# Optimization experiments

Measured on AMD Instinct MI355X. Metric: run time of the kernel, lower is better.

Reference implementation:

```python
import jax, jax.numpy as jnp
import numpy as np

B = 8192        # batch
OBS = 256       # obs_dim
ACT = 32        # action_dim -> output is 2*ACT (mu, log_std)
HID = 512       # hidden_dim
P = 8           # number of base policies (experts)
LOG_STD_MIN, LOG_STD_MAX = -5.0, 2.0


def setup_inputs() -> dict:
    key = jax.random.key(0)
    ks = jax.random.split(key, 14)
    s = 0.05
    return {
        "obs": jax.random.normal(ks[0], (B, OBS), dtype=jnp.float32),
        # gate network: obs -> HID -> HID -> P (softmax)
        "gw0": jax.random.normal(ks[1], (HID, OBS), dtype=jnp.float32) * s,
        "gb0": jnp.zeros((HID,), dtype=jnp.float32),
        "gw1": jax.random.normal(ks[2], (HID, HID), dtype=jnp.float32) * s,
        "gb1": jnp.zeros((HID,), dtype=jnp.float32),
        "gw2": jax.random.normal(ks[3], (P, HID), dtype=jnp.float32) * s,
        "gb2": jnp.zeros((P,), dtype=jnp.float32),
        # stacked expert (base-policy) trunk params, hidden_depth=2
        "ew0": jax.random.normal(ks[4], (P, HID, OBS), dtype=jnp.float32) * s,
        "eb0": jax.random.normal(ks[5], (P, HID), dtype=jnp.float32) * s,
        "ew1": jax.random.normal(ks[6], (P, HID, HID), dtype=jnp.float32) * s,
        "eb1": jax.random.normal(ks[7], (P, HID), dtype=jnp.float32) * s,
        "ew2": jax.random.normal(ks[8], (P, 2 * ACT, HID), dtype=jnp.float32) * s,
        "eb2": jax.random.normal(ks[9], (P, 2 * ACT), dtype=jnp.float32) * s,
    }


def _blend_linear(blend, W, b, x):
    # Math identical to: W_new = reshape(blend @ flatten(W,1)); bmm(W_new, x) + blend @ b
    # Contracted in the efficient order (per-expert GEMM then blend): [B,P,out] intermediate.
    y = jnp.einsum('bp,poi,bi->bo', blend, W, x, optimize=True)
    return y + blend @ b


def reference(obs, gw0, gb0, gw1, gb1, gw2, gb2, ew0, eb0, ew1, eb1, ew2, eb2):
    # gate network with softmax output
    h = jax.nn.relu(obs @ gw0.T + gb0)
    h = jax.nn.relu(h @ gw1.T + gb1)
    blend = jax.nn.softmax(h @ gw2.T + gb2, axis=-1)  # [B, P]

    # blended per-sample MLP (hidden_depth = 2)
    x = jax.nn.relu(_blend_linear(blend, ew0, eb0, obs))
    x = jax.nn.relu(_blend_linear(blend, ew1, eb1, x))
    x = _blend_linear(blend, ew2, eb2, x)  # [B, 2*ACT]

    mu, log_std = jnp.split(x, 2, axis=-1)
    log_std = jnp.tanh(log_std)
    log_std = LOG_STD_MIN + 0.5 * (LOG_STD_MAX - LOG_STD_MIN) * (log_std + 1.0)
    std = jnp.exp(log_std)
    # dist = SquashedNormal(mu, std); return its defining tensors
    return jnp.concatenate([mu, std], axis=-1)
```

## Files before the change

kernel.cpp:

```cpp
#include <hip/hip_runtime.h>
#include <hip/hip_bf16.h>
#include <cstdint>
#include <cstddef>

#define B_DIM   8192
#define OBS_DIM 256
#define ACT_DIM 32
#define HID_DIM 512
#define NEXPERT 8

typedef __attribute__((ext_vector_type(4))) float        f32x4;
typedef __attribute__((ext_vector_type(8))) short        s16x8;
typedef __attribute__((ext_vector_type(4))) unsigned int u32x4;

__device__ __forceinline__ unsigned cvt_pk_bf16(float lo, float hi) {
    unsigned r;
    asm("v_cvt_pk_bf16_f32 %0, %1, %2" : "=v"(r) : "v"(lo), "v"(hi));
    return r;
}
__device__ __forceinline__ float bf16_lo_f32(unsigned u) { return __uint_as_float(u << 16); }
__device__ __forceinline__ float bf16_hi_f32(unsigned u) { return __uint_as_float(u & 0xffff0000u); }

struct CvtArgs {
    const float*    s[7];
    unsigned short* d[7];
    int             nb[7];
};

__global__ __launch_bounds__(256) void cvt_multi(CvtArgs a) {
    int bid = blockIdx.x;
    int seg = 0, base = 0;
    while (seg < 6 && bid >= base + a.nb[seg]) { base += a.nb[seg]; ++seg; }
    int local = (bid - base) * 256 + threadIdx.x;
    const f32x4* s = (const f32x4*)a.s[seg];
    f32x4 v0 = s[local * 2 + 0];
    f32x4 v1 = s[local * 2 + 1];
    u32x4 o;
    o[0] = cvt_pk_bf16(v0[0], v0[1]);
    o[1] = cvt_pk_bf16(v0[2], v0[3]);
    o[2] = cvt_pk_bf16(v1[0], v1[1]);
    o[3] = cvt_pk_bf16(v1[2], v1[3]);
    ((u32x4*)a.d[seg])[local] = o;
}

__global__ __launch_bounds__(256) void gate_softmax(const unsigned short* __restrict__ h1,
                                                    const unsigned short* __restrict__ gw2,
                                                    const float* __restrict__ gb2,
                                                    float* __restrict__ blend) {
    const int lane = threadIdx.x & 63;
    const int wid  = threadIdx.x >> 6;
    const int row  = blockIdx.x * 4 + wid;

    u32x4 xv = *(const u32x4*)(h1 + (size_t)row * HID_DIM + lane * 8);
    float x[8];
#pragma unroll
    for (int j = 0; j < 4; ++j) {
        unsigned u   = xv[j];
        x[2 * j]     = bf16_lo_f32(u);
        x[2 * j + 1] = bf16_hi_f32(u);
    }
    float s[NEXPERT];
#pragma unroll
    for (int pp = 0; pp < NEXPERT; ++pp) {
        u32x4 wv = *(const u32x4*)(gw2 + (size_t)pp * HID_DIM + lane * 8);
        float d  = 0.f;
#pragma unroll
        for (int j = 0; j < 4; ++j) {
            unsigned u = wv[j];
            d += x[2 * j] * bf16_lo_f32(u);
            d += x[2 * j + 1] * bf16_hi_f32(u);
        }
        s[pp] = d;
    }
#pragma unroll
    for (int off = 1; off < 64; off <<= 1) {
#pragma unroll
        for (int pp = 0; pp < NEXPERT; ++pp) s[pp] += __shfl_xor(s[pp], off);
    }
    if (lane == 0) {
        float l[NEXPERT], m = -1e30f;
#pragma unroll
        for (int pp = 0; pp < NEXPERT; ++pp) { l[pp] = s[pp] + gb2[pp]; m = fmaxf(m, l[pp]); }
        float sum = 0.f;
#pragma unroll
        for (int pp = 0; pp < NEXPERT; ++pp) { l[pp] = __expf(l[pp] - m); sum += l[pp]; }
        float inv = 1.f / sum;
#pragma unroll
        for (int pp = 0; pp < NEXPERT; ++pp) blend[(size_t)row * NEXPERT + pp] = l[pp] * inv;
    }
}

template <int KIN, int NOUT>
__global__ __launch_bounds__(256, 2) void gemm_gate(const unsigned short* __restrict__ A,
                                                    const unsigned short* __restrict__ W,
                                                    const float* __restrict__ bias,
                                                    unsigned short* __restrict__ outb) {
    constexpr int BM = 128, BN = 64, BK = 64;
    constexpr int NT = KIN / BK;

    __shared__ unsigned short sA[2][BM * BK];
    __shared__ unsigned short sB[2][BN * BK];

    const int t    = threadIdx.x;
    const int lane = t & 63;
    const int wid  = t >> 6;
    const int wm   = wid >> 1, wn = wid & 1;
    const int m0   = blockIdx.x * BM;
    const int n0   = blockIdx.y * BN;

    auto stage = [&](int tile, int buf) {
        const int ks = tile * BK;
        const unsigned short* Wp = W + (size_t)n0 * KIN + ks;
#pragma unroll
        for (int c = 0; c < 2; ++c) {
            const int ch  = c * 256 + t;
            const int row = ch >> 3;
            const int gs  = (ch & 7) ^ (row & 7);
            __builtin_amdgcn_global_load_lds(
                (const __attribute__((address_space(1))) unsigned int*)(Wp + (size_t)row * KIN + gs * 8),
                (__attribute__((address_space(3))) unsigned int*)(&sB[buf][ch * 8]), 16, 0, 0);
        }
        const unsigned short* Ap = A + (size_t)m0 * KIN + ks;
#pragma unroll
        for (int c = 0; c < 4; ++c) {
            const int ch  = c * 256 + t;
            const int row = ch >> 3;
            const int gs  = (ch & 7) ^ (row & 7);
            __builtin_amdgcn_global_load_lds(
                (const __attribute__((address_space(1))) unsigned int*)(Ap + (size_t)row * KIN + gs * 8),
                (__attribute__((address_space(3))) unsigned int*)(&sA[buf][ch * 8]), 16, 0, 0);
        }
    };

    f32x4 acc[4][2];
#pragma unroll
    for (int i = 0; i < 4; ++i)
#pragma unroll
        for (int j = 0; j < 2; ++j) acc[i][j] = {0.f, 0.f, 0.f, 0.f};

    stage(0, 0);
    __syncthreads();
    int cur = 0;

#pragma unroll 1
    for (int tile = 0; tile < NT; ++tile) {
        if (tile + 1 < NT) stage(tile + 1, cur ^ 1);

#pragma unroll
        for (int kk = 0; kk < BK; kk += 32) {
            const int kb = kk + ((lane >> 4) << 3);
            s16x8 af[4], bfr[2];
#pragma unroll
            for (int mf = 0; mf < 4; ++mf) {
                const int row = wm * 64 + mf * 16 + (lane & 15);
                const int idx = (row * BK + kb) ^ ((row & 7) << 3);
                af[mf] = *(const s16x8*)(&sA[cur][idx]);
            }
#pragma unroll
            for (int nf = 0; nf < 2; ++nf) {
                const int row = wn * 32 + nf * 16 + (lane & 15);
                const int idx = (row * BK + kb) ^ ((row & 7) << 3);
                bfr[nf] = *(const s16x8*)(&sB[cur][idx]);
            }
#pragma unroll
            for (int mf = 0; mf < 4; ++mf)
#pragma unroll
                for (int nf = 0; nf < 2; ++nf)
                    acc[mf][nf] = __builtin_amdgcn_mfma_f32_16x16x32_bf16(af[mf], bfr[nf],
                                                                          acc[mf][nf], 0, 0, 0);
        }
        __syncthreads();
        cur ^= 1;
    }

    const int cn = lane & 15;
    const int rb = (lane >> 4) << 2;
#pragma unroll
    for (int nf = 0; nf < 2; ++nf) {
        const int gn   = n0 + wn * 32 + nf * 16 + cn;
        const float bv = bias[gn];
#pragma unroll
        for (int mf = 0; mf < 4; ++mf) {
#pragma unroll
            for (int r = 0; r < 4; ++r) {
                const int gm = m0 + wm * 64 + mf * 16 + rb + r;
                float v = fmaxf(acc[mf][nf][r] + bv, 0.f);
                outb[(size_t)gm * NOUT + gn] = (unsigned short)(cvt_pk_bf16(v, v) & 0xffffu);
            }
        }
    }
}

template <int KIN, int NOUT, int BN, int TPB, int EPI>
__global__ __launch_bounds__(256, 2) void gemm_moe_db(const unsigned short* __restrict__ A,
                                                      const unsigned short* __restrict__ W,
                                                      const float* __restrict__ blend,
                                                      const float* __restrict__ ebias,
                                                      unsigned short* __restrict__ outb,
                                                      float* __restrict__ part) {
    constexpr int BM  = 128, BK = 64;
    constexpr int NF  = BN / 32;
    constexpr int TPE = KIN / BK;
    constexpr int ET  = (TPB >= TPE) ? TPE : TPB;
    static_assert((TPB % TPE == 0) || (TPE % TPB == 0), "split/expert alignment");
    static_assert(EPI == 0 || TPB == TPE, "EPI1 assumes exactly one expert/block");

    __shared__ unsigned short sA[2][BM * BK];
    __shared__ unsigned short sB[2][BN * BK];
    __shared__ float          sBl[BM][12];

    const int t    = threadIdx.x;
    const int lane = t & 63;
    const int wid  = t >> 6;
    const int wm   = wid >> 1, wn = wid & 1;
    const int m0   = blockIdx.x * BM;
    const int n0   = blockIdx.y * BN;
    const int sp   = blockIdx.z;
    const unsigned gbase = (unsigned)sp * TPB;

    const int cn = lane & 15;
    const int rb = (lane >> 4) << 2;

    {
        const int r = t >> 1;
        const int c = (t & 1) * 4;
        *(f32x4*)&sBl[r][c] = *(const f32x4*)(blend + (size_t)(m0 + r) * NEXPERT + c);
    }

    auto stage = [&](int tile, int buf) {
        const unsigned g  = gbase + (unsigned)tile;
        const unsigned p  = g / TPE;
        const unsigned ko = (g % TPE) * BK;
        const unsigned short* Wp = W + ((size_t)p * NOUT + n0) * KIN + ko;
#pragma unroll
        for (int c = 0; c < BN / 32; ++c) {
            const int ch  = c * 256 + t;
            const int row = ch >> 3;
            const int gs  = (ch & 7) ^ (row & 7);
            __builtin_amdgcn_global_load_lds(
                (const __attribute__((address_space(1))) unsigned int*)(Wp + (size_t)row * KIN + gs * 8),
                (__attribute__((address_space(3))) unsigned int*)(&sB[buf][ch * 8]), 16, 0, 0);
        }
        const unsigned short* Ap = A + (size_t)m0 * KIN + ko;
#pragma unroll
        for (int c = 0; c < 4; ++c) {
            const int ch  = c * 256 + t;
            const int row = ch >> 3;
            const int gs  = (ch & 7) ^ (row & 7);
            __builtin_amdgcn_global_load_lds(
                (const __attribute__((address_space(1))) unsigned int*)(Ap + (size_t)row * KIN + gs * 8),
                (__attribute__((address_space(3))) unsigned int*)(&sA[buf][ch * 8]), 16, 0, 0);
        }
    };

    f32x4 mast[4][NF], eacc[4][NF];
#pragma unroll
    for (int i = 0; i < 4; ++i)
#pragma unroll
        for (int j = 0; j < NF; ++j) {
            mast[i][j] = {0.f, 0.f, 0.f, 0.f};
            eacc[i][j] = {0.f, 0.f, 0.f, 0.f};
        }

    stage(0, 0);
    int cur = 0;

#pragma unroll 1
    for (int tile = 0; tile < TPB; ++tile) {
        if (tile + 1 < TPB) {
            stage(tile + 1, cur ^ 1);
            if constexpr (BN == 128) {
                asm volatile("s_waitcnt vmcnt(8)" ::: "memory");
            } else {
                asm volatile("s_waitcnt vmcnt(6)" ::: "memory");
            }
        } else {
            asm volatile("s_waitcnt vmcnt(0)" ::: "memory");
        }
        __builtin_amdgcn_s_barrier();
        __builtin_amdgcn_sched_barrier(0);

#pragma unroll
        for (int kk = 0; kk < BK; kk += 32) {
            const int kb = kk + ((lane >> 4) << 3);
            s16x8 af[4], bfr[NF];
#pragma unroll
            for (int mf = 0; mf < 4; ++mf) {
                const int row = wm * 64 + mf * 16 + (lane & 15);
                const int idx = (row * BK + kb) ^ ((row & 7) << 3);
                af[mf] = *(const s16x8*)(&sA[cur][idx]);
            }
#pragma unroll
            for (int nf = 0; nf < NF; ++nf) {
                const int row = wn * (BN / 2) + nf * 16 + (lane & 15);
                const int idx = (row * BK + kb) ^ ((row & 7) << 3);
                bfr[nf] = *(const s16x8*)(&sB[cur][idx]);
            }
#pragma unroll
            for (int mf = 0; mf < 4; ++mf)
#pragma unroll
                for (int nf = 0; nf < NF; ++nf)
                    eacc[mf][nf] = __builtin_amdgcn_mfma_f32_16x16x32_bf16(af[mf], bfr[nf],
                                                                           eacc[mf][nf], 0, 0, 0);
        }

        if (((tile + 1) & (ET - 1)) == 0) {
            const unsigned p = (gbase + (unsigned)tile) / TPE;
#pragma unroll
            for (int mf = 0; mf < 4; ++mf) {
#pragma unroll
                for (int r = 0; r < 4; ++r) {
                    const int lr = wm * 64 + mf * 16 + rb + r;
                    const float bl = sBl[lr][p];
#pragma unroll
                    for (int nf = 0; nf < NF; ++nf) {
                        mast[mf][nf][r] += bl * eacc[mf][nf][r];
                        eacc[mf][nf][r] = 0.f;
                    }
                }
            }
        }

        asm volatile("s_waitcnt lgkmcnt(0)" ::: "memory");
        __builtin_amdgcn_s_barrier();
        cur ^= 1;
    }

    if constexpr (EPI == 0) {
#pragma unroll
        for (int nf = 0; nf < NF; ++nf) {
            const int gn = n0 + wn * (BN / 2) + nf * 16 + cn;
            float ebv[NEXPERT];
#pragma unroll
            for (int pp = 0; pp < NEXPERT; ++pp) ebv[pp] = ebias[pp * NOUT + gn];
#pragma unroll
            for (int mf = 0; mf < 4; ++mf) {
#pragma unroll
                for (int r = 0; r < 4; ++r) {
                    const int lr = wm * 64 + mf * 16 + rb + r;
                    float bb = 0.f;
#pragma unroll
                    for (int pp = 0; pp < NEXPERT; ++pp) bb += sBl[lr][pp] * ebv[pp];
                    const float v = fmaxf(mast[mf][nf][r] + bb, 0.f);
                    outb[(size_t)(m0 + lr) * NOUT + gn] =
                        (unsigned short)(cvt_pk_bf16(v, v) & 0xffffu);
                }
            }
        }
    } else {
        float* dst = part + (size_t)sp * B_DIM * NOUT;
#pragma unroll
        for (int mf = 0; mf < 4; ++mf) {
#pragma unroll
            for (int r = 0; r < 4; ++r) {
                const int lr = wm * 64 + mf * 16 + rb + r;
#pragma unroll
                for (int nf = 0; nf < NF; ++nf) {
                    const int gn = n0 + wn * (BN / 2) + nf * 16 + cn;
                    dst[(size_t)(m0 + lr) * NOUT + gn] = mast[mf][nf][r];
                }
            }
        }
    }
}

__global__ __launch_bounds__(256) void reduce8_head(const float* __restrict__ part,
                                                    const float* __restrict__ blend,
                                                    const float* __restrict__ eb2,
                                                    float* __restrict__ out) {
    const int tid = blockIdx.x * 256 + threadIdx.x;
    const int row = tid >> 3;
    const int c0  = (tid & 7) << 3;

    float res[8] = {0.f, 0.f, 0.f, 0.f, 0.f, 0.f, 0.f, 0.f};
#pragma unroll
    for (int sp = 0; sp < 8; ++sp) {
        const f32x4* ps = (const f32x4*)(part + ((size_t)sp * B_DIM + row) * 64 + c0);
        const f32x4 a = ps[0], b = ps[1];
#pragma unroll
        for (int j = 0; j < 4; ++j) { res[j] += a[j]; res[4 + j] += b[j]; }
    }
    const f32x4* bl = (const f32x4*)(blend + (size_t)row * NEXPERT);
    const f32x4 b0 = bl[0], b1 = bl[1];
    const float blv[8] = {b0[0], b0[1], b0[2], b0[3], b1[0], b1[1], b1[2], b1[3]};
#pragma unroll
    for (int pp = 0; pp < NEXPERT; ++pp) {
        const f32x4* e = (const f32x4*)(eb2 + (size_t)pp * 64 + c0);
        const f32x4 e0 = e[0], e1 = e[1];
#pragma unroll
        for (int j = 0; j < 4; ++j) {
            res[j]     += blv[pp] * e0[j];
            res[4 + j] += blv[pp] * e1[j];
        }
    }
    f32x4 o0, o1;
#pragma unroll
    for (int j = 0; j < 8; ++j) {
        const int col = c0 + j;
        float v = res[j];
        if (col >= ACT_DIM) {
            const float vc = fminf(fmaxf(v, -15.f), 15.f);
            const float e2 = __expf(2.f * vc);
            const float th = (e2 - 1.f) / (e2 + 1.f);
            v = __expf(-1.5f + 3.5f * th);
        }
        if (j < 4) o0[j] = v; else o1[j - 4] = v;
    }
    f32x4* dst = (f32x4*)(out + (size_t)row * 64 + c0);
    dst[0] = o0;
    dst[1] = o1;
}

extern "C" void kernel_launch(void* const* d_in, const int* in_sizes, int n_in,
                              void* d_out, int out_size, void* d_ws, size_t ws_size,
                              hipStream_t stream) {
    const float* obs = (const float*)d_in[0];
    const float* gw0 = (const float*)d_in[1];
    const float* gb0 = (const float*)d_in[2];
    const float* gw1 = (const float*)d_in[3];
    const float* gb1 = (const float*)d_in[4];
    const float* gw2 = (const float*)d_in[5];
    const float* gb2 = (const float*)d_in[6];
    const float* ew0 = (const float*)d_in[7];
    const float* eb0 = (const float*)d_in[8];
    const float* ew1 = (const float*)d_in[9];
    const float* eb1 = (const float*)d_in[10];
    const float* ew2 = (const float*)d_in[11];
    const float* eb2 = (const float*)d_in[12];

    char* w = (char*)d_ws;
    auto alloc = [&](size_t bytes) {
        char* r = w;
        w += (bytes + 255) & ~(size_t)255;
        return r;
    };
    unsigned short* obs_bf = (unsigned short*)alloc((size_t)B_DIM * OBS_DIM * 2);
    unsigned short* gw0_bf = (unsigned short*)alloc((size_t)HID_DIM * OBS_DIM * 2);
    unsigned short* gw1_bf = (unsigned short*)alloc((size_t)HID_DIM * HID_DIM * 2);
    unsigned short* gw2_bf = (unsigned short*)alloc((size_t)NEXPERT * HID_DIM * 2);
    unsigned short* ew0_bf = (unsigned short*)alloc((size_t)NEXPERT * HID_DIM * OBS_DIM * 2);
    unsigned short* ew1_bf = (unsigned short*)alloc((size_t)NEXPERT * HID_DIM * HID_DIM * 2);
    unsigned short* ew2_bf = (unsigned short*)alloc((size_t)NEXPERT * 2 * ACT_DIM * HID_DIM * 2);
    unsigned short* h0     = (unsigned short*)alloc((size_t)B_DIM * HID_DIM * 2);
    unsigned short* h1     = (unsigned short*)alloc((size_t)B_DIM * HID_DIM * 2);
    float*          blend  = (float*)alloc((size_t)B_DIM * NEXPERT * 4);
    float*          part   = (float*)alloc((size_t)8 * B_DIM * 64 * 4);

    CvtArgs ca;
    ca.s[0] = obs; ca.d[0] = obs_bf; ca.nb[0] = (B_DIM * OBS_DIM / 8) / 256;
    ca.s[1] = gw0; ca.d[1] = gw0_bf; ca.nb[1] = (HID_DIM * OBS_DIM / 8) / 256;
    ca.s[2] = gw1; ca.d[2] = gw1_bf; ca.nb[2] = (HID_DIM * HID_DIM / 8) / 256;
    ca.s[3] = gw2; ca.d[3] = gw2_bf; ca.nb[3] = (NEXPERT * HID_DIM / 8) / 256;
    ca.s[4] = ew0; ca.d[4] = ew0_bf; ca.nb[4] = (NEXPERT * HID_DIM * OBS_DIM / 8) / 256;
    ca.s[5] = ew1; ca.d[5] = ew1_bf; ca.nb[5] = (NEXPERT * HID_DIM * HID_DIM / 8) / 256;
    ca.s[6] = ew2; ca.d[6] = ew2_bf; ca.nb[6] = (NEXPERT * 64 * HID_DIM / 8) / 256;
    int total_blocks = 0;
    for (int i = 0; i < 7; ++i) total_blocks += ca.nb[i];
    cvt_multi<<<total_blocks, 256, 0, stream>>>(ca);

    gemm_gate<OBS_DIM, HID_DIM><<<dim3(B_DIM / 128, HID_DIM / 64), 256, 0, stream>>>(
        obs_bf, gw0_bf, gb0, h0);
    gemm_gate<HID_DIM, HID_DIM><<<dim3(B_DIM / 128, HID_DIM / 64), 256, 0, stream>>>(
        h0, gw1_bf, gb1, h1);
    gate_softmax<<<B_DIM / 4, 256, 0, stream>>>(h1, gw2_bf, gb2, blend);

    gemm_moe_db<OBS_DIM, HID_DIM, 128, 32, 0>
        <<<dim3(B_DIM / 128, HID_DIM / 128, 1), 256, 0, stream>>>(
            obs_bf, ew0_bf, blend, eb0, h0, nullptr);

    gemm_moe_db<HID_DIM, HID_DIM, 128, 64, 0>
        <<<dim3(B_DIM / 128, HID_DIM / 128, 1), 256, 0, stream>>>(
            h0, ew1_bf, blend, eb1, h1, nullptr);

    gemm_moe_db<HID_DIM, 64, 64, 8, 1>
        <<<dim3(B_DIM / 128, 1, 8), 256, 0, stream>>>(
            h1, ew2_bf, blend, nullptr, nullptr, part);
    reduce8_head<<<B_DIM * 8 / 256, 256, 0, stream>>>(part, blend, eb2, (float*)d_out);
}
```

Before: 232.8 us.

## Split-K the first two blended expert GEMMs with separate reduce+bias+relu kernel

The two hidden-layer MoE GEMMs now split their expert K-loop across two grid slices (z=2), each writing fp32 partials, followed by a new reduction kernel that sums partials, adds the blended bias, applies ReLU and packs to bf16. The aim is more blocks in flight (only 256 blocks before) to fill the GPU. In exchange it writes and reads large fp32 partial buffers (2x8192x512) and adds two extra launches. The static_assert forbidding EPI1 with multi-expert tiles is removed, which relies on the partial epilogue being valid when a block spans several experts.

New measurement: 210.3 us. -9.7%, faster.

```diff
diff --git a/kernel.cpp b/kernel.cpp
--- a/kernel.cpp
+++ b/kernel.cpp
@@ -203,7 +203,6 @@
     constexpr int TPE = KIN / BK;
     constexpr int ET  = (TPB >= TPE) ? TPE : TPB;
     static_assert((TPB % TPE == 0) || (TPE % TPB == 0), "split/expert alignment");
-    static_assert(EPI == 0 || TPB == TPE, "EPI1 assumes exactly one expert/block");
 
     __shared__ unsigned short sA[2][BM * BK];
     __shared__ unsigned short sB[2][BN * BK];
@@ -362,6 +361,43 @@
             }
         }
     }
+}
+
+template <int NS>
+__global__ __launch_bounds__(256) void reduceN_relu(const float* __restrict__ part,
+                                                    const float* __restrict__ blend,
+                                                    const float* __restrict__ eb,
+                                                    unsigned short* __restrict__ out) {
+    const int tid = blockIdx.x * 256 + threadIdx.x;
+    const int row = tid >> 6;
+    const int c0  = (tid & 63) << 3;
+
+    float res[8] = {0.f, 0.f, 0.f, 0.f, 0.f, 0.f, 0.f, 0.f};
+#pragma unroll
+    for (int s = 0; s < NS; ++s) {
+        const f32x4* ps = (const f32x4*)(part + ((size_t)s * B_DIM + row) * HID_DIM + c0);
+        const f32x4 a = ps[0], b = ps[1];
+#pragma unroll
+        for (int j = 0; j < 4; ++j) { res[j] += a[j]; res[4 + j] += b[j]; }
+    }
+    const f32x4* bl = (const f32x4*)(blend + (size_t)row * NEXPERT);
+    const f32x4 b0 = bl[0], b1 = bl[1];
+    const float blv[8] = {b0[0], b0[1], b0[2], b0[3], b1[0], b1[1], b1[2], b1[3]};
+#pragma unroll
+    for (int pp = 0; pp < NEXPERT; ++pp) {
+        const f32x4* e = (const f32x4*)(eb + (size_t)pp * HID_DIM + c0);
+        const f32x4 e0 = e[0], e1 = e[1];
+#pragma unroll
+        for (int j = 0; j < 4; ++j) {
+            res[j]     += blv[pp] * e0[j];
+            res[4 + j] += blv[pp] * e1[j];
+        }
+    }
+    u32x4 o;
+#pragma unroll
+    for (int j = 0; j < 4; ++j)
+        o[j] = cvt_pk_bf16(fmaxf(res[2 * j], 0.f), fmaxf(res[2 * j + 1], 0.f));
+    *(u32x4*)(out + (size_t)row * HID_DIM + c0) = o;
 }
 
 __global__ __launch_bounds__(256) void reduce8_head(const float* __restrict__ part,
@@ -444,7 +480,7 @@
     unsigned short* h0     = (unsigned short*)alloc((size_t)B_DIM * HID_DIM * 2);
     unsigned short* h1     = (unsigned short*)alloc((size_t)B_DIM * HID_DIM * 2);
     float*          blend  = (float*)alloc((size_t)B_DIM * NEXPERT * 4);
-    float*          part   = (float*)alloc((size_t)8 * B_DIM * 64 * 4);
+    float*          part   = (float*)alloc((size_t)2 * B_DIM * HID_DIM * 4);
 
     CvtArgs ca;
     ca.s[0] = obs; ca.d[0] = obs_bf; ca.nb[0] = (B_DIM * OBS_DIM / 8) / 256;
@@ -464,13 +500,15 @@
         h0, gw1_bf, gb1, h1);
     gate_softmax<<<B_DIM / 4, 256, 0, stream>>>(h1, gw2_bf, gb2, blend);
 
-    gemm_moe_db<OBS_DIM, HID_DIM, 128, 32, 0>
-        <<<dim3(B_DIM / 128, HID_DIM / 128, 1), 256, 0, stream>>>(
-            obs_bf, ew0_bf, blend, eb0, h0, nullptr);
-
-    gemm_moe_db<HID_DIM, HID_DIM, 128, 64, 0>
-        <<<dim3(B_DIM / 128, HID_DIM / 128, 1), 256, 0, stream>>>(
-            h0, ew1_bf, blend, eb1, h1, nullptr);
+    gemm_moe_db<OBS_DIM, HID_DIM, 128, 16, 1>
+        <<<dim3(B_DIM / 128, HID_DIM / 128, 2), 256, 0, stream>>>(
+            obs_bf, ew0_bf, blend, nullptr, nullptr, part);
+    reduceN_relu<2><<<B_DIM * 64 / 256, 256, 0, stream>>>(part, blend, eb0, h0);
+
+    gemm_moe_db<HID_DIM, HID_DIM, 128, 32, 1>
+        <<<dim3(B_DIM / 128, HID_DIM / 128, 2), 256, 0, stream>>>(
+            h0, ew1_bf, blend, nullptr, nullptr, part);
+    reduceN_relu<2><<<B_DIM * 64 / 256, 256, 0, stream>>>(part, blend, eb1, h1);
 
     gemm_moe_db<HID_DIM, 64, 64, 8, 1>
         <<<dim3(B_DIM / 128, 1, 8), 256, 0, stream>>>(
```
